# Optimization experiments

Measured on AMD Instinct MI355X. Metric: run time of the kernel, lower is better.

## Reference

```python
import jax, jax.numpy as jnp
import numpy as np

N, C, K = 400000, 32, 27
EPS = 1e-5


def sparse_conv(feats, W, nbr, mask):
    # feats [N,Cin], W [K,Cin,Cout], nbr [N,K] int, mask [N,K] bool
    g = feats[nbr] * mask[..., None]          # gather: [N,K,Cin]
    return jnp.einsum('nki,kio->no', g, W)    # per-offset GEMM + scatter-accumulate


def batchnorm(x, gamma, beta):
    # MinkowskiBatchNorm over all active points (axis 0), training-mode stats
    mean = jnp.mean(x, axis=0)
    var = jnp.var(x, axis=0)
    return (x - mean) * jax.lax.rsqrt(var + EPS) * gamma + beta


def setup_inputs() -> dict:
    key = jax.random.key(0)
    ks = jax.random.split(key, 8)
    feats = jax.random.normal(ks[0], (N, C), dtype=jnp.float32)
    nbr = jax.random.randint(ks[1], (N, K), 0, N, dtype=jnp.int32)
    mask = jax.random.randint(ks[2], (N, K), 0, 2, dtype=jnp.int32).astype(bool)
    scale = 1.0 / np.sqrt(K * C)
    W1 = jax.random.normal(ks[3], (K, C, C), dtype=jnp.float32) * scale
    W2 = jax.random.normal(ks[4], (K, C, C), dtype=jnp.float32) * scale
    gamma1 = jnp.ones((C,), jnp.float32)
    beta1 = jnp.zeros((C,), jnp.float32)
    gamma2 = jnp.ones((C,), jnp.float32)
    beta2 = jnp.zeros((C,), jnp.float32)
    return {"feats": feats, "W1": W1, "gamma1": gamma1, "beta1": beta1,
            "W2": W2, "gamma2": gamma2, "beta2": beta2,
            "nbr": nbr, "mask": mask}


def reference(feats, W1, gamma1, beta1, W2, gamma2, beta2, nbr, mask):
    h = sparse_conv(feats, W1, nbr, mask)
    h = jax.nn.relu(batchnorm(h, gamma1, beta1))
    h = sparse_conv(h, W2, nbr, mask)
    h = batchnorm(h, gamma2, beta2)
    # in_ch == out_ch -> identity residual (no downsample branch)
    return jax.nn.relu(h + feats)
```

## Files before the change

kernel.cpp:

```cpp
#include <hip/hip_runtime.h>

#define NPTS 400000
#define KOFF 27

typedef __attribute__((ext_vector_type(8))) __bf16 bf16x8;
typedef __attribute__((ext_vector_type(4))) float v4f;

__device__ __forceinline__ float bf2f(unsigned short u) {
  union { unsigned int i; float f; } v; v.i = ((unsigned int)u) << 16; return v.f;
}
__device__ __forceinline__ unsigned short f2bf(float f) {
  union { float f; unsigned int i; } v; v.f = f;
  unsigned int x = v.i;
  return (unsigned short)((x + 0x7FFFu + ((x >> 16) & 1u)) >> 16);
}

__global__ void prep_feats(const float* __restrict__ feats, unsigned short* __restrict__ Xb,
                           unsigned short* __restrict__ H1, float* __restrict__ statszero) {
  int idx = blockIdx.x * 256 + threadIdx.x;
  const float4* f4 = (const float4*)feats;
  float4 a = f4[2 * idx], b = f4[2 * idx + 1];
  union { unsigned short u[8]; uint4 v; } p;
  p.u[0] = f2bf(a.x); p.u[1] = f2bf(a.y); p.u[2] = f2bf(a.z); p.u[3] = f2bf(a.w);
  p.u[4] = f2bf(b.x); p.u[5] = f2bf(b.y); p.u[6] = f2bf(b.z); p.u[7] = f2bf(b.w);
  ((uint4*)Xb)[idx] = p.v;
  if (blockIdx.x == 0) {
    if (threadIdx.x < 32) {
      Xb[(size_t)NPTS * 32 + threadIdx.x] = 0;
      H1[(size_t)NPTS * 32 + threadIdx.x] = 0;
    }
    if (threadIdx.x < 128) statszero[threadIdx.x] = 0.f;
  }
}

__global__ void prep_nbr(const int* __restrict__ nbr, const int* __restrict__ mask,
                         int* __restrict__ nbrT) {
  __shared__ int tile[256 * KOFF];
  int p0 = blockIdx.x * 256;
  int cnt = (NPTS - p0 < 256) ? (NPTS - p0) : 256;
  int total = cnt * KOFF;
  for (int i = threadIdx.x; i < total; i += 256) {
    int j = nbr[(size_t)p0 * KOFF + i];
    int mk = mask[(size_t)p0 * KOFF + i];
    tile[i] = (mk != 0) ? j : NPTS;
  }
  __syncthreads();
  int t = threadIdx.x;
  if (t < cnt) {
    #pragma unroll
    for (int k = 0; k < KOFF; ++k)
      nbrT[(size_t)k * NPTS + p0 + t] = tile[t * KOFF + k];
  }
}

__global__ void prep_w(const float* __restrict__ W1, const float* __restrict__ W2,
                       unsigned short* __restrict__ WL1, unsigned short* __restrict__ WL2) {
  int idx = blockIdx.x * 256 + threadIdx.x;
  if (idx >= KOFF * 1024) return;
  int k = idx >> 10, r = idx & 1023;
  int h = r >> 9, rr = r & 511;
  int lane = rr >> 3, j = rr & 7;
  int i_ch = (lane >> 4) * 8 + j;
  int o_ch = h * 16 + (lane & 15);
  int src = k * 1024 + i_ch * 32 + o_ch;
  WL1[idx] = f2bf(W1[src]);
  WL2[idx] = f2bf(W2[src]);
}

__global__ __launch_bounds__(1024, 8) void conv_mfma16(
    const unsigned short* __restrict__ X,
    const int* __restrict__ nbrT,
    const unsigned short* __restrict__ WL,
    unsigned short* __restrict__ Hout,
    float* __restrict__ stats)
{
  __shared__ unsigned char wlds[KOFF * 2048];
  __shared__ float redS[16][32];
  __shared__ float redQ[16][32];

  const int tid = threadIdx.x;
  {
    const uint4* src = (const uint4*)WL;
    uint4* dst = (uint4*)wlds;
    for (int i = tid; i < KOFF * 128; i += 1024) dst[i] = src[i];
  }
  __syncthreads();

  const int lane = tid & 63;
  const int wv   = tid >> 6;
  const int m    = lane & 15;
  const int q    = lane >> 4;
  const int n0   = blockIdx.x * 256 + wv * 16;
  const bool active = (n0 < NPTS);

  v4f acc0 = {0.f, 0.f, 0.f, 0.f};
  v4f acc1 = {0.f, 0.f, 0.f, 0.f};
  float s0 = 0.f, s1 = 0.f, qq0 = 0.f, qq1 = 0.f;

  if (active) {
    const int* nbp = nbrT + n0 + m;
    const unsigned short* xq = X + q * 8;
    const bf16x8* wfrag = (const bf16x8*)wlds;
    int nb = nbp[0];
    #pragma unroll 3
    for (int k = 0; k < KOFF; ++k) {
      int nb_next = (k < KOFF - 1) ? nbp[(k + 1) * NPTS] : 0;
      bf16x8 a  = *(const bf16x8*)(xq + (size_t)nb * 32);
      bf16x8 b0 = wfrag[(k * 2 + 0) * 64 + lane];
      bf16x8 b1 = wfrag[(k * 2 + 1) * 64 + lane];
      acc0 = __builtin_amdgcn_mfma_f32_16x16x32_bf16(a, b0, acc0, 0, 0, 0);
      acc1 = __builtin_amdgcn_mfma_f32_16x16x32_bf16(a, b1, acc1, 0, 0, 0);
      nb = nb_next;
    }
    #pragma unroll
    for (int r = 0; r < 4; ++r) {
      float v0 = acc0[r], v1 = acc1[r];
      s0 += v0; s1 += v1; qq0 += v0 * v0; qq1 += v1 * v1;
      size_t pt = (size_t)(n0 + q * 4 + r);
      Hout[pt * 32 + m]      = f2bf(v0);
      Hout[pt * 32 + 16 + m] = f2bf(v1);
    }
  }
  s0  += __shfl_xor(s0, 16);  s0  += __shfl_xor(s0, 32);
  s1  += __shfl_xor(s1, 16);  s1  += __shfl_xor(s1, 32);
  qq0 += __shfl_xor(qq0, 16); qq0 += __shfl_xor(qq0, 32);
  qq1 += __shfl_xor(qq1, 16); qq1 += __shfl_xor(qq1, 32);
  if (lane < 16) {
    redS[wv][m] = s0; redS[wv][m + 16] = s1;
    redQ[wv][m] = qq0; redQ[wv][m + 16] = qq1;
  }
  __syncthreads();
  if (tid < 64) {
    int t = tid & 31;
    float a = 0.f;
    if (tid < 32) { for (int w = 0; w < 16; ++w) a += redS[w][t]; }
    else          { for (int w = 0; w < 16; ++w) a += redQ[w][t]; }
    atomicAdd(&stats[tid], a);
  }
}

__global__ void bn_relu_fused(unsigned short* __restrict__ H, const float* __restrict__ stats,
                              const float* __restrict__ gamma, const float* __restrict__ beta) {
  __shared__ float sb[64];
  if (threadIdx.x < 32) {
    int t = threadIdx.x;
    float mean = stats[t] * (1.f / NPTS);
    float var  = stats[t + 32] * (1.f / NPTS) - mean * mean;
    float rstd = rsqrtf(var + 1e-5f);
    float sc = gamma[t] * rstd;
    sb[t] = sc; sb[t + 32] = beta[t] - mean * sc;
  }
  __syncthreads();
  int idx = blockIdx.x * 256 + threadIdx.x;
  uint4 v = ((uint4*)H)[idx];
  union { uint4 v; unsigned short u[8]; } p; p.v = v;
  int baseo = (idx * 8) & 31;
  #pragma unroll
  for (int j = 0; j < 8; ++j) {
    float f = bf2f(p.u[j]);
    f = fmaxf(f * sb[baseo + j] + sb[32 + baseo + j], 0.f);
    p.u[j] = f2bf(f);
  }
  ((uint4*)H)[idx] = p.v;
}

__global__ void bn_res_relu_out(const unsigned short* __restrict__ H2, const float* __restrict__ feats,
                                const float* __restrict__ stats, const float* __restrict__ gamma,
                                const float* __restrict__ beta, float* __restrict__ out) {
  __shared__ float sb[64];
  if (threadIdx.x < 32) {
    int t = threadIdx.x;
    float mean = stats[t] * (1.f / NPTS);
    float var  = stats[t + 32] * (1.f / NPTS) - mean * mean;
    float rstd = rsqrtf(var + 1e-5f);
    float sc = gamma[t] * rstd;
    sb[t] = sc; sb[t + 32] = beta[t] - mean * sc;
  }
  __syncthreads();
  int idx = blockIdx.x * 256 + threadIdx.x;
  uint4 v = ((const uint4*)H2)[idx];
  union { uint4 v; unsigned short u[8]; } p; p.v = v;
  int baseo = (idx * 8) & 31;
  const float4* f4 = (const float4*)feats;
  float4 fa = f4[2 * idx], fb = f4[2 * idx + 1];
  float4 o0, o1;
  float* fav = (float*)&fa; float* fbv = (float*)&fb;
  float* o0v = (float*)&o0; float* o1v = (float*)&o1;
  #pragma unroll
  for (int j = 0; j < 4; ++j)
    o0v[j] = fmaxf(bf2f(p.u[j]) * sb[baseo + j] + sb[32 + baseo + j] + fav[j], 0.f);
  #pragma unroll
  for (int j = 0; j < 4; ++j)
    o1v[j] = fmaxf(bf2f(p.u[4 + j]) * sb[baseo + 4 + j] + sb[32 + baseo + 4 + j] + fbv[j], 0.f);
  ((float4*)out)[2 * idx] = o0;
  ((float4*)out)[2 * idx + 1] = o1;
}

extern "C" void kernel_launch(void* const* d_in, const int* in_sizes, int n_in,
                              void* d_out, int out_size, void* d_ws, size_t ws_size,
                              hipStream_t stream) {
  const float* feats  = (const float*)d_in[0];
  const float* W1     = (const float*)d_in[1];
  const float* gamma1 = (const float*)d_in[2];
  const float* beta1  = (const float*)d_in[3];
  const float* W2     = (const float*)d_in[4];
  const float* gamma2 = (const float*)d_in[5];
  const float* beta2  = (const float*)d_in[6];
  const int*   nbr    = (const int*)d_in[7];
  const int*   mask   = (const int*)d_in[8];

  char* ws = (char*)d_ws;
  const size_t XB = ((size_t)(NPTS + 1) * 32 * 2 + 255) & ~(size_t)255;
  unsigned short* Xb   = (unsigned short*)(ws);
  unsigned short* H1   = (unsigned short*)(ws + XB);
  int*            nbrT = (int*)(ws + 2 * XB);
  size_t off = 2 * XB + (size_t)KOFF * NPTS * 4;
  unsigned short* WL1 = (unsigned short*)(ws + off); off += KOFF * 1024 * 2;
  unsigned short* WL2 = (unsigned short*)(ws + off); off += KOFF * 1024 * 2;
  float* stats1 = (float*)(ws + off); off += 256;
  float* stats2 = (float*)(ws + off); off += 256;
  unsigned short* H2 = Xb;

  prep_feats<<<6250, 256, 0, stream>>>(feats, Xb, H1, stats1);
  prep_nbr<<<1563, 256, 0, stream>>>(nbr, mask, nbrT);
  prep_w<<<108, 256, 0, stream>>>(W1, W2, WL1, WL2);

  conv_mfma16<<<1563, 1024, 0, stream>>>(Xb, nbrT, WL1, H1, stats1);
  bn_relu_fused<<<6250, 256, 0, stream>>>(H1, stats1, gamma1, beta1);

  conv_mfma16<<<1563, 1024, 0, stream>>>(H1, nbrT, WL2, H2, stats2);
  bn_res_relu_out<<<6250, 256, 0, stream>>>(H2, feats, stats2, gamma2, beta2, (float*)d_out);
}
```

Baseline: 455.6 us.

## Batch neighbor gathers in conv, shrink blocks, fuse prep kernels into one

The conv kernel now preloads all 27 neighbor indices into registers and issues the feature gathers in batches of nine, double-buffered, ahead of the MFMAs. This raises memory-level parallelism and hides gather latency. Blocks drop from 1024 to 512 threads, which removes the tail guard since 3125*128 covers all points exactly. The three prep kernels are merged into one launch to cut launch overhead. The cost is much higher register pressure, up to 18 bf16x8 fragments plus 27 indices, which may reduce occupancy.

```diff
diff --git a/kernel.cpp b/kernel.cpp
--- a/kernel.cpp
+++ b/kernel.cpp
@@ -15,8 +15,13 @@
   return (unsigned short)((x + 0x7FFFu + ((x >> 16) & 1u)) >> 16);
 }
 
-__global__ void prep_feats(const float* __restrict__ feats, unsigned short* __restrict__ Xb,
-                           unsigned short* __restrict__ H1, float* __restrict__ statszero) {
+__global__ void prep_all(const float* __restrict__ feats, unsigned short* __restrict__ Xb,
+                         unsigned short* __restrict__ H1, float* __restrict__ statszero,
+                         const int* __restrict__ nbr, const int* __restrict__ mask,
+                         int* __restrict__ nbrT,
+                         const float* __restrict__ W1, const float* __restrict__ W2,
+                         unsigned short* __restrict__ WL1, unsigned short* __restrict__ WL2) {
+  __shared__ int tile[256 * KOFF];
   int idx = blockIdx.x * 256 + threadIdx.x;
   const float4* f4 = (const float4*)feats;
   float4 a = f4[2 * idx], b = f4[2 * idx + 1];
@@ -31,43 +36,38 @@
     }
     if (threadIdx.x < 128) statszero[threadIdx.x] = 0.f;
   }
-}
-
-__global__ void prep_nbr(const int* __restrict__ nbr, const int* __restrict__ mask,
-                         int* __restrict__ nbrT) {
-  __shared__ int tile[256 * KOFF];
-  int p0 = blockIdx.x * 256;
-  int cnt = (NPTS - p0 < 256) ? (NPTS - p0) : 256;
-  int total = cnt * KOFF;
-  for (int i = threadIdx.x; i < total; i += 256) {
-    int j = nbr[(size_t)p0 * KOFF + i];
-    int mk = mask[(size_t)p0 * KOFF + i];
-    tile[i] = (mk != 0) ? j : NPTS;
-  }
-  __syncthreads();
-  int t = threadIdx.x;
-  if (t < cnt) {
-    #pragma unroll
-    for (int k = 0; k < KOFF; ++k)
-      nbrT[(size_t)k * NPTS + p0 + t] = tile[t * KOFF + k];
-  }
-}
-
-__global__ void prep_w(const float* __restrict__ W1, const float* __restrict__ W2,
-                       unsigned short* __restrict__ WL1, unsigned short* __restrict__ WL2) {
-  int idx = blockIdx.x * 256 + threadIdx.x;
-  if (idx >= KOFF * 1024) return;
-  int k = idx >> 10, r = idx & 1023;
-  int h = r >> 9, rr = r & 511;
-  int lane = rr >> 3, j = rr & 7;
-  int i_ch = (lane >> 4) * 8 + j;
-  int o_ch = h * 16 + (lane & 15);
-  int src = k * 1024 + i_ch * 32 + o_ch;
-  WL1[idx] = f2bf(W1[src]);
-  WL2[idx] = f2bf(W2[src]);
-}
-
-__global__ __launch_bounds__(1024, 8) void conv_mfma16(
+  if (blockIdx.x < 1563) {
+    int p0 = blockIdx.x * 256;
+    int cnt = (NPTS - p0 < 256) ? (NPTS - p0) : 256;
+    int total = cnt * KOFF;
+    for (int i = threadIdx.x; i < total; i += 256) {
+      int j = nbr[(size_t)p0 * KOFF + i];
+      int mk = mask[(size_t)p0 * KOFF + i];
+      tile[i] = (mk != 0) ? j : NPTS;
+    }
+    __syncthreads();
+    int t = threadIdx.x;
+    if (t < cnt) {
+      #pragma unroll
+      for (int k = 0; k < KOFF; ++k)
+        nbrT[(size_t)k * NPTS + p0 + t] = tile[t * KOFF + k];
+    }
+  } else if (blockIdx.x < 1563 + 108) {
+    int widx = (blockIdx.x - 1563) * 256 + threadIdx.x;
+    if (widx < KOFF * 1024) {
+      int k = widx >> 10, r = widx & 1023;
+      int h = r >> 9, rr = r & 511;
+      int lane = rr >> 3, j = rr & 7;
+      int i_ch = (lane >> 4) * 8 + j;
+      int o_ch = h * 16 + (lane & 15);
+      int src = k * 1024 + i_ch * 32 + o_ch;
+      WL1[widx] = f2bf(W1[src]);
+      WL2[widx] = f2bf(W2[src]);
+    }
+  }
+}
+
+__global__ __launch_bounds__(512, 4) void conv_mfma16(
     const unsigned short* __restrict__ X,
     const int* __restrict__ nbrT,
     const unsigned short* __restrict__ WL,
@@ -75,14 +75,18 @@
     float* __restrict__ stats)
 {
   __shared__ unsigned char wlds[KOFF * 2048];
-  __shared__ float redS[16][32];
-  __shared__ float redQ[16][32];
+  __shared__ float redS[8][32];
+  __shared__ float redQ[8][32];
 
   const int tid = threadIdx.x;
   {
     const uint4* src = (const uint4*)WL;
     uint4* dst = (uint4*)wlds;
-    for (int i = tid; i < KOFF * 128; i += 1024) dst[i] = src[i];
+    #pragma unroll
+    for (int i = 0; i < 7; ++i) {
+      int ii = i * 512 + tid;
+      if (ii < KOFF * 128) dst[ii] = src[ii];
+    }
   }
   __syncthreads();
 
@@ -90,36 +94,59 @@
   const int wv   = tid >> 6;
   const int m    = lane & 15;
   const int q    = lane >> 4;
-  const int n0   = blockIdx.x * 256 + wv * 16;
-  const bool active = (n0 < NPTS);
+  const int n0   = blockIdx.x * 128 + wv * 16;
+
+  const int* nbp = nbrT + n0 + m;
+  int nb[KOFF];
+  #pragma unroll
+  for (int k = 0; k < KOFF; ++k) nb[k] = nbp[k * NPTS];
+
+  const unsigned short* xq = X + q * 8;
+  const bf16x8* wfrag = (const bf16x8*)wlds;
 
   v4f acc0 = {0.f, 0.f, 0.f, 0.f};
   v4f acc1 = {0.f, 0.f, 0.f, 0.f};
+
+  bf16x8 A0[9], A1[9];
+  #pragma unroll
+  for (int k = 0; k < 9; ++k) A0[k] = *(const bf16x8*)(xq + (size_t)nb[k] * 32);
+  #pragma unroll
+  for (int k = 0; k < 9; ++k) A1[k] = *(const bf16x8*)(xq + (size_t)nb[9 + k] * 32);
+
+  #pragma unroll
+  for (int k = 0; k < 9; ++k) {
+    bf16x8 b0 = wfrag[(k * 2 + 0) * 64 + lane];
+    bf16x8 b1 = wfrag[(k * 2 + 1) * 64 + lane];
+    acc0 = __builtin_amdgcn_mfma_f32_16x16x32_bf16(A0[k], b0, acc0, 0, 0, 0);
+    acc1 = __builtin_amdgcn_mfma_f32_16x16x32_bf16(A0[k], b1, acc1, 0, 0, 0);
+  }
+  #pragma unroll
+  for (int k = 0; k < 9; ++k) A0[k] = *(const bf16x8*)(xq + (size_t)nb[18 + k] * 32);
+  #pragma unroll
+  for (int k = 0; k < 9; ++k) {
+    int kk = 9 + k;
+    bf16x8 b0 = wfrag[(kk * 2 + 0) * 64 + lane];
+    bf16x8 b1 = wfrag[(kk * 2 + 1) * 64 + lane];
+    acc0 = __builtin_amdgcn_mfma_f32_16x16x32_bf16(A1[k], b0, acc0, 0, 0, 0);
+    acc1 = __builtin_amdgcn_mfma_f32_16x16x32_bf16(A1[k], b1, acc1, 0, 0, 0);
+  }
+  #pragma unroll
+  for (int k = 0; k < 9; ++k) {
+    int kk = 18 + k;
+    bf16x8 b0 = wfrag[(kk * 2 + 0) * 64 + lane];
+    bf16x8 b1 = wfrag[(kk * 2 + 1) * 64 + lane];
+    acc0 = __builtin_amdgcn_mfma_f32_16x16x32_bf16(A0[k], b0, acc0, 0, 0, 0);
+    acc1 = __builtin_amdgcn_mfma_f32_16x16x32_bf16(A0[k], b1, acc1, 0, 0, 0);
+  }
+
   float s0 = 0.f, s1 = 0.f, qq0 = 0.f, qq1 = 0.f;
-
-  if (active) {
-    const int* nbp = nbrT + n0 + m;
-    const unsigned short* xq = X + q * 8;
-    const bf16x8* wfrag = (const bf16x8*)wlds;
-    int nb = nbp[0];
-    #pragma unroll 3
-    for (int k = 0; k < KOFF; ++k) {
-      int nb_next = (k < KOFF - 1) ? nbp[(k + 1) * NPTS] : 0;
-      bf16x8 a  = *(const bf16x8*)(xq + (size_t)nb * 32);
-      bf16x8 b0 = wfrag[(k * 2 + 0) * 64 + lane];
-      bf16x8 b1 = wfrag[(k * 2 + 1) * 64 + lane];
-      acc0 = __builtin_amdgcn_mfma_f32_16x16x32_bf16(a, b0, acc0, 0, 0, 0);
-      acc1 = __builtin_amdgcn_mfma_f32_16x16x32_bf16(a, b1, acc1, 0, 0, 0);
-      nb = nb_next;
-    }
-    #pragma unroll
-    for (int r = 0; r < 4; ++r) {
-      float v0 = acc0[r], v1 = acc1[r];
-      s0 += v0; s1 += v1; qq0 += v0 * v0; qq1 += v1 * v1;
-      size_t pt = (size_t)(n0 + q * 4 + r);
-      Hout[pt * 32 + m]      = f2bf(v0);
-      Hout[pt * 32 + 16 + m] = f2bf(v1);
-    }
+  #pragma unroll
+  for (int r = 0; r < 4; ++r) {
+    float v0 = acc0[r], v1 = acc1[r];
+    s0 += v0; s1 += v1; qq0 += v0 * v0; qq1 += v1 * v1;
+    size_t pt = (size_t)(n0 + q * 4 + r);
+    Hout[pt * 32 + m]      = f2bf(v0);
+    Hout[pt * 32 + 16 + m] = f2bf(v1);
   }
   s0  += __shfl_xor(s0, 16);  s0  += __shfl_xor(s0, 32);
   s1  += __shfl_xor(s1, 16);  s1  += __shfl_xor(s1, 32);
@@ -133,8 +160,8 @@
   if (tid < 64) {
     int t = tid & 31;
     float a = 0.f;
-    if (tid < 32) { for (int w = 0; w < 16; ++w) a += redS[w][t]; }
-    else          { for (int w = 0; w < 16; ++w) a += redQ[w][t]; }
+    if (tid < 32) { for (int w = 0; w < 8; ++w) a += redS[w][t]; }
+    else          { for (int w = 0; w < 8; ++w) a += redQ[w][t]; }
     atomicAdd(&stats[tid], a);
   }
 }
@@ -221,13 +248,11 @@
   float* stats2 = (float*)(ws + off); off += 256;
   unsigned short* H2 = Xb;
 
-  prep_feats<<<6250, 256, 0, stream>>>(feats, Xb, H1, stats1);
-  prep_nbr<<<1563, 256, 0, stream>>>(nbr, mask, nbrT);
-  prep_w<<<108, 256, 0, stream>>>(W1, W2, WL1, WL2);
-
-  conv_mfma16<<<1563, 1024, 0, stream>>>(Xb, nbrT, WL1, H1, stats1);
+  prep_all<<<6250, 256, 0, stream>>>(feats, Xb, H1, stats1, nbr, mask, nbrT, W1, W2, WL1, WL2);
+
+  conv_mfma16<<<3125, 512, 0, stream>>>(Xb, nbrT, WL1, H1, stats1);
   bn_relu_fused<<<6250, 256, 0, stream>>>(H1, stats1, gamma1, beta1);
 
-  conv_mfma16<<<1563, 1024, 0, stream>>>(H1, nbrT, WL2, H2, stats2);
+  conv_mfma16<<<3125, 512, 0, stream>>>(H1, nbrT, WL2, H2, stats2);
   bn_res_relu_out<<<6250, 256, 0, stream>>>(H2, feats, stats2, gamma2, beta2, (float*)d_out);
 }
```

New measurement: 423.9 us. 7.0% less time.
